# Performance work log

Hardware: AMD Instinct MI355X
Metric: run time of the kernel (lower is better)

Reference implementation:

```python
import jax, jax.numpy as jnp
import numpy as np

E = 800000
NUM_RADIAL = 6
HIDDEN = 128
OUT = 128
NUM_NODES = 50000


def setup_inputs() -> dict:
    key = jax.random.key(0)
    ks = jax.random.split(key, 12)
    x = jax.random.normal(ks[0], (E, HIDDEN), dtype=jnp.float32)
    rbf = jax.random.uniform(ks[1], (E, NUM_RADIAL), dtype=jnp.float32)
    i = jax.random.randint(ks[2], (E,), 0, NUM_NODES, dtype=jnp.int64)
    s = 1.0 / np.sqrt(HIDDEN)
    W_rbf = jax.random.normal(ks[3], (HIDDEN, NUM_RADIAL), dtype=jnp.float32) / np.sqrt(NUM_RADIAL)
    W1 = jax.random.normal(ks[4], (HIDDEN, HIDDEN), dtype=jnp.float32) * s
    b1 = jnp.zeros((HIDDEN,), dtype=jnp.float32)
    W2 = jax.random.normal(ks[5], (HIDDEN, HIDDEN), dtype=jnp.float32) * s
    b2 = jnp.zeros((HIDDEN,), dtype=jnp.float32)
    W3 = jax.random.normal(ks[6], (HIDDEN, HIDDEN), dtype=jnp.float32) * s
    b3 = jnp.zeros((HIDDEN,), dtype=jnp.float32)
    W_out = jax.random.normal(ks[7], (OUT, HIDDEN), dtype=jnp.float32) * s
    return {"x": x, "rbf": rbf, "i": i, "num_nodes": NUM_NODES,
            "W_rbf": W_rbf, "W1": W1, "b1": b1, "W2": W2, "b2": b2,
            "W3": W3, "b3": b3, "W_out": W_out}


def reference(x, rbf, i, num_nodes, W_rbf, W1, b1, W2, b2, W3, b3, W_out):
    # edge-wise: lin_rbf(rbf) * x, then scatter-add to nodes
    m = (rbf @ W_rbf.T) * x                      # [E, H]
    h = jax.ops.segment_sum(m, i, num_segments=num_nodes)  # [N, H]
    # MLP stack with swish activation
    h = jax.nn.silu(h @ W1.T + b1)
    h = jax.nn.silu(h @ W2.T + b2)
    h = jax.nn.silu(h @ W3.T + b3)
    return h @ W_out.T                           # [N, OUT]
```

## Files before the change

### kernel.cpp

```cpp
#include <hip/hip_runtime.h>

#define H 128
#define NR 6
#define MT 128
#define HS 136

typedef __attribute__((ext_vector_type(8))) short short8_t;
typedef __attribute__((ext_vector_type(4))) float f32x4;

__device__ __forceinline__ float silu_f(float v) {
    return v / (1.0f + __expf(-v));
}

__device__ __forceinline__ unsigned short bf16_rne(float f) {
    unsigned u = __float_as_uint(f);
    u += 0x7FFF + ((u >> 16) & 1);
    return (unsigned short)(u >> 16);
}
__device__ __forceinline__ float bf16_to_f(unsigned short s) {
    return __uint_as_float(((unsigned)s) << 16);
}

__global__ __launch_bounds__(256) void hist_k(const int* __restrict__ idx,
                                              int* __restrict__ counts, int E) {
    int i = blockIdx.x * 256 + threadIdx.x;
    if (i < E) atomicAdd(&counts[idx[i]], 1);
}

__global__ __launch_bounds__(1024) void scan_k(const int* __restrict__ counts,
                                               int* __restrict__ offsets, int N) {
    __shared__ int wsum[16];
    __shared__ int runv;
    const int tid = threadIdx.x, lane = tid & 63, wv = tid >> 6;
    if (tid == 0) runv = 0;
    __syncthreads();
    for (int base = 0; base < N; base += 1024) {
        const int j = base + tid;
        const int v_in = (j < N) ? counts[j] : 0;
        int v = v_in;
        #pragma unroll
        for (int d = 1; d < 64; d <<= 1) {
            int u = __shfl_up(v, d);
            if (lane >= d) v += u;
        }
        if (lane == 63) wsum[wv] = v;
        __syncthreads();
        if (tid < 16) {
            int s = wsum[tid];
            #pragma unroll
            for (int d = 1; d < 16; d <<= 1) {
                int u = __shfl_up(s, d);
                if (tid >= d) s += u;
            }
            wsum[tid] = s;
        }
        __syncthreads();
        const int wexcl = (wv == 0) ? 0 : wsum[wv - 1];
        const int r0 = runv;
        if (j < N) offsets[j] = r0 + wexcl + (v - v_in);
        const int tot = wsum[15];
        __syncthreads();
        if (tid == 0) runv = r0 + tot;
        __syncthreads();
    }
    if (tid == 0) offsets[N] = runv;
}

__global__ __launch_bounds__(256) void fill_k(const int* __restrict__ idx,
                                              const int* __restrict__ offsets,
                                              int* __restrict__ cursor,
                                              int* __restrict__ elist, int E) {
    int i = blockIdx.x * 256 + threadIdx.x;
    if (i < E) {
        int node = idx[i];
        int pos = atomicAdd(&cursor[node], 1);
        elist[offsets[node] + pos] = i;
    }
}

__global__ __launch_bounds__(256) void wsplit_k(
    const float* __restrict__ W1, const float* __restrict__ W2,
    const float* __restrict__ W3, const float* __restrict__ Wo,
    unsigned short* __restrict__ dst)
{
    const float* W = (blockIdx.y == 0) ? W1 : (blockIdx.y == 1) ? W2
                   : (blockIdx.y == 2) ? W3 : Wo;
    unsigned short* hi = dst + (size_t)blockIdx.y * 2 * H * H;
    unsigned short* lo = hi + H * H;
    const int i = (blockIdx.x * 256 + threadIdx.x) * 4;
    if (i < H * H) {
        const float4 v = *(const float4*)(W + i);
        ushort4 h4, l4;
        h4.x = bf16_rne(v.x); l4.x = bf16_rne(v.x - bf16_to_f(h4.x));
        h4.y = bf16_rne(v.y); l4.y = bf16_rne(v.y - bf16_to_f(h4.y));
        h4.z = bf16_rne(v.z); l4.z = bf16_rne(v.z - bf16_to_f(h4.z));
        h4.w = bf16_rne(v.w); l4.w = bf16_rne(v.w - bf16_to_f(h4.w));
        *(ushort4*)&hi[i] = h4;
        *(ushort4*)&lo[i] = l4;
    }
}


__device__ __forceinline__ void stage_w_pre(const unsigned short* __restrict__ g,
        unsigned short* w_hi, unsigned short* w_lo, int t)
{
    const unsigned short* hi_g = g;
    const unsigned short* lo_g = g + H * H;
    for (int i = t * 8; i < H * H; i += 4096) {
        const int c = i >> 7, k = i & 127;
        *(short8_t*)&w_hi[c * HS + k] = *(const short8_t*)&hi_g[i];
        *(short8_t*)&w_lo[c * HS + k] = *(const short8_t*)&lo_g[i];
    }
}

__device__ __forceinline__ void compute_gemm(
    const unsigned short* h_hi, const unsigned short* h_lo,
    const unsigned short* w_hi, const unsigned short* w_lo,
    const float* bl, int wv, int lr, int quad, f32x4 (&acc)[8])
{
    short8_t a_hi[4], a_lo[4];
    const int row = wv * 16 + lr;
    #pragma unroll
    for (int kb = 0; kb < 4; ++kb) {
        const int off = row * HS + kb * 32 + quad * 8;
        a_hi[kb] = *(const short8_t*)&h_hi[off];
        a_lo[kb] = *(const short8_t*)&h_lo[off];
    }
    #pragma unroll
    for (int ct = 0; ct < 8; ct += 2) {
        const int c0 = ct * 16 + lr, c1 = (ct + 1) * 16 + lr;
        const float bb0 = bl[c0], bb1 = bl[c1];
        f32x4 A0 = {bb0, bb0, bb0, bb0}, A1 = {bb1, bb1, bb1, bb1};
        short8_t b0h[4], b0l[4], b1h[4], b1l[4];
        #pragma unroll
        for (int kb = 0; kb < 4; ++kb) {
            const int o0 = c0 * HS + kb * 32 + quad * 8;
            const int o1 = c1 * HS + kb * 32 + quad * 8;
            b0h[kb] = *(const short8_t*)&w_hi[o0];
            b0l[kb] = *(const short8_t*)&w_lo[o0];
            b1h[kb] = *(const short8_t*)&w_hi[o1];
            b1l[kb] = *(const short8_t*)&w_lo[o1];
        }
        #pragma unroll
        for (int kb = 0; kb < 4; ++kb) {
            A0 = __builtin_amdgcn_mfma_f32_16x16x32_bf16(a_hi[kb], b0h[kb], A0, 0, 0, 0);
            A1 = __builtin_amdgcn_mfma_f32_16x16x32_bf16(a_hi[kb], b1h[kb], A1, 0, 0, 0);
            A0 = __builtin_amdgcn_mfma_f32_16x16x32_bf16(a_hi[kb], b0l[kb], A0, 0, 0, 0);
            A1 = __builtin_amdgcn_mfma_f32_16x16x32_bf16(a_hi[kb], b1l[kb], A1, 0, 0, 0);
            A0 = __builtin_amdgcn_mfma_f32_16x16x32_bf16(a_lo[kb], b0h[kb], A0, 0, 0, 0);
            A1 = __builtin_amdgcn_mfma_f32_16x16x32_bf16(a_lo[kb], b1h[kb], A1, 0, 0, 0);
        }
        acc[ct] = A0;
        acc[ct + 1] = A1;
    }
}

__device__ __forceinline__ void epilogue_silu(
    unsigned short* h_hi, unsigned short* h_lo,
    f32x4 (&acc)[8], int wv, int lr, int quad)
{
    #pragma unroll
    for (int ct = 0; ct < 8; ++ct)
        #pragma unroll
        for (int r = 0; r < 4; ++r) {
            const int row = wv * 16 + quad * 4 + r;
            const int col = ct * 16 + lr;
            const float v = silu_f(acc[ct][r]);
            const unsigned short hi = bf16_rne(v);
            h_hi[row * HS + col] = hi;
            h_lo[row * HS + col] = bf16_rne(v - bf16_to_f(hi));
        }
}

__global__ __launch_bounds__(512, 2) void fused_mlp(
    const float* __restrict__ x, const float* __restrict__ rbf,
    const float* __restrict__ W_rbf,
    const int* __restrict__ offsets, const int* __restrict__ elist,
    const unsigned short* __restrict__ wsp,
    const float* __restrict__ b1, const float* __restrict__ b2,
    const float* __restrict__ b3,
    float* __restrict__ out, int N)
{
    __shared__ unsigned short h_hi[H * HS], h_lo[H * HS];
    __shared__ unsigned short w_hi[H * HS], w_lo[H * HS];
    __shared__ float bl[H];

    const int t = threadIdx.x;
    const int lane = t & 63;
    const int wv = t >> 6;
    const int lr = lane & 15;
    const int quad = lane >> 4;
    const int sub = lane >> 5;
    const int l32 = lane & 31;
    const int row0 = blockIdx.x * MT;

    const float4* wp = (const float4*)(W_rbf + l32 * 24);
    const float4 w0 = wp[0], w1 = wp[1], w2 = wp[2], w3 = wp[3],
                 w4 = wp[4], w5 = wp[5];
    const float wr[4][NR] = {
        {w0.x, w0.y, w0.z, w0.w, w1.x, w1.y},
        {w1.z, w1.w, w2.x, w2.y, w2.z, w2.w},
        {w3.x, w3.y, w3.z, w3.w, w4.x, w4.y},
        {w4.z, w4.w, w5.x, w5.y, w5.z, w5.w}};

    for (int i = 0; i < 16; ++i) {
        const int node = row0 + wv * 16 + i;
        float4 ga = make_float4(0.f, 0.f, 0.f, 0.f);
        if (node < N) {
            const int beg = offsets[node], end = offsets[node + 1];
            for (int base = beg; base < end; base += 64) {
                const int cnt = min(64, end - base);
                const int e_lane = (lane < cnt) ? elist[base + lane] : 0;
                for (int p = 0; p < cnt; p += 8) {
                    int ev[4];
                    bool val[4];
                    float4 xv[4];
                    float2 rv[4][3];
                    #pragma unroll
                    for (int q = 0; q < 4; ++q) {
                        const int slot = p + 2 * q + sub;
                        val[q] = slot < cnt;
                        ev[q] = __shfl(e_lane, val[q] ? slot : cnt - 1);
                    }
                    #pragma unroll
                    for (int q = 0; q < 4; ++q) {
                        const size_t e = (size_t)ev[q];
                        xv[q] = *(const float4*)(x + e * H + l32 * 4);
                        const float2* rp = (const float2*)(rbf + e * NR);
                        rv[q][0] = rp[0]; rv[q][1] = rp[1]; rv[q][2] = rp[2];
                    }
                    #pragma unroll
                    for (int q = 0; q < 4; ++q) {
                        if (!val[q]) continue;
                        const float rr[NR] = {rv[q][0].x, rv[q][0].y, rv[q][1].x,
                                              rv[q][1].y, rv[q][2].x, rv[q][2].y};
                        float s0 = 0.f, s1 = 0.f, s2 = 0.f, s3 = 0.f;
                        #pragma unroll
                        for (int j = 0; j < NR; ++j) {
                            s0 += rr[j] * wr[0][j];
                            s1 += rr[j] * wr[1][j];
                            s2 += rr[j] * wr[2][j];
                            s3 += rr[j] * wr[3][j];
                        }
                        ga.x += s0 * xv[q].x;
                        ga.y += s1 * xv[q].y;
                        ga.z += s2 * xv[q].z;
                        ga.w += s3 * xv[q].w;
                    }
                }
            }
            ga.x += __shfl_xor(ga.x, 32);
            ga.y += __shfl_xor(ga.y, 32);
            ga.z += __shfl_xor(ga.z, 32);
            ga.w += __shfl_xor(ga.w, 32);
        }
        if (sub == 0) {
            ushort4 h4, l4;
            h4.x = bf16_rne(ga.x); l4.x = bf16_rne(ga.x - bf16_to_f(h4.x));
            h4.y = bf16_rne(ga.y); l4.y = bf16_rne(ga.y - bf16_to_f(h4.y));
            h4.z = bf16_rne(ga.z); l4.z = bf16_rne(ga.z - bf16_to_f(h4.z));
            h4.w = bf16_rne(ga.w); l4.w = bf16_rne(ga.w - bf16_to_f(h4.w));
            const int off = (wv * 16 + i) * HS + l32 * 4;
            *(ushort4*)&h_hi[off] = h4;
            *(ushort4*)&h_lo[off] = l4;
        }
    }

    stage_w_pre(wsp, w_hi, w_lo, t);
    if (t < H) bl[t] = b1[t];
    __syncthreads();

    f32x4 acc[8];

    compute_gemm(h_hi, h_lo, w_hi, w_lo, bl, wv, lr, quad, acc);
    __syncthreads();
    epilogue_silu(h_hi, h_lo, acc, wv, lr, quad);
    stage_w_pre(wsp + 32768, w_hi, w_lo, t);
    if (t < H) bl[t] = b2[t];
    __syncthreads();

    compute_gemm(h_hi, h_lo, w_hi, w_lo, bl, wv, lr, quad, acc);
    __syncthreads();
    epilogue_silu(h_hi, h_lo, acc, wv, lr, quad);
    stage_w_pre(wsp + 65536, w_hi, w_lo, t);
    if (t < H) bl[t] = b3[t];
    __syncthreads();

    compute_gemm(h_hi, h_lo, w_hi, w_lo, bl, wv, lr, quad, acc);
    __syncthreads();
    epilogue_silu(h_hi, h_lo, acc, wv, lr, quad);
    stage_w_pre(wsp + 98304, w_hi, w_lo, t);
    if (t < H) bl[t] = 0.f;
    __syncthreads();

    compute_gemm(h_hi, h_lo, w_hi, w_lo, bl, wv, lr, quad, acc);

    #pragma unroll
    for (int ct = 0; ct < 8; ++ct)
        #pragma unroll
        for (int r = 0; r < 4; ++r) {
            const int row = row0 + wv * 16 + quad * 4 + r;
            if (row < N) out[(size_t)row * H + ct * 16 + lr] = acc[ct][r];
        }
}

static inline size_t align256(size_t v) { return (v + 255) & ~(size_t)255; }

extern "C" void kernel_launch(void* const* d_in, const int* in_sizes, int n_in,
                              void* d_out, int out_size, void* d_ws, size_t ws_size,
                              hipStream_t stream) {
    const float* x     = (const float*)d_in[0];
    const float* rbf   = (const float*)d_in[1];
    const int*   idx   = (const int*)d_in[2];
    const float* W_rbf = (const float*)d_in[4];
    const float* W1    = (const float*)d_in[5];
    const float* b1    = (const float*)d_in[6];
    const float* W2    = (const float*)d_in[7];
    const float* b2    = (const float*)d_in[8];
    const float* W3    = (const float*)d_in[9];
    const float* b3    = (const float*)d_in[10];
    const float* Wo    = (const float*)d_in[11];
    float* out = (float*)d_out;

    const int E = in_sizes[0] / H;
    const int N = out_size / H;

    char* ws = (char*)d_ws;
    size_t off = 0;
    unsigned short* wsp = (unsigned short*)(ws + off);
    off = align256(off + (size_t)4 * 2 * H * H * sizeof(unsigned short));
    int* counts  = (int*)(ws + off);   off = align256(off + (size_t)N * 4);
    int* cursor  = (int*)(ws + off);   off = align256(off + (size_t)N * 4);
    int* offsets = (int*)(ws + off);   off = align256(off + (size_t)(N + 1) * 4);
    int* elist   = (int*)(ws + off);   off = align256(off + (size_t)E * 4);

    hipMemsetAsync(counts, 0, (char*)offsets - (char*)counts, stream);

    wsplit_k<<<dim3(16, 4), 256, 0, stream>>>(W1, W2, W3, Wo, wsp);
    hist_k<<<(E + 255) / 256, 256, 0, stream>>>(idx, counts, E);
    scan_k<<<1, 1024, 0, stream>>>(counts, offsets, N);
    fill_k<<<(E + 255) / 256, 256, 0, stream>>>(idx, offsets, cursor, elist, E);
    fused_mlp<<<(N + MT - 1) / MT, 512, 0, stream>>>(
        x, rbf, W_rbf, offsets, elist, wsp, b1, b2, b3, out, N);
}
```

Before: 774.4 us.

## Balance edge gather across half-waves with LDS atomics and vectorize CSR build kernels

```diff
diff --git a/kernel.cpp b/kernel.cpp
--- a/kernel.cpp
+++ b/kernel.cpp
@@ -23,8 +23,16 @@
 
 __global__ __launch_bounds__(256) void hist_k(const int* __restrict__ idx,
                                               int* __restrict__ counts, int E) {
-    int i = blockIdx.x * 256 + threadIdx.x;
-    if (i < E) atomicAdd(&counts[idx[i]], 1);
+    const int i0 = (blockIdx.x * 256 + threadIdx.x) * 4;
+    if (i0 + 3 < E) {
+        const int4 v = *(const int4*)(idx + i0);
+        atomicAdd(&counts[v.x], 1);
+        atomicAdd(&counts[v.y], 1);
+        atomicAdd(&counts[v.z], 1);
+        atomicAdd(&counts[v.w], 1);
+    } else {
+        for (int i = i0; i < E; ++i) atomicAdd(&counts[idx[i]], 1);
+    }
 }
 
 __global__ __launch_bounds__(1024) void scan_k(const int* __restrict__ counts,
@@ -34,16 +42,23 @@
     const int tid = threadIdx.x, lane = tid & 63, wv = tid >> 6;
     if (tid == 0) runv = 0;
     __syncthreads();
-    for (int base = 0; base < N; base += 1024) {
-        const int j = base + tid;
-        const int v_in = (j < N) ? counts[j] : 0;
-        int v = v_in;
+    for (int base = 0; base < N; base += 4096) {
+        const int j0 = base + tid * 4;
+        int4 v = make_int4(0, 0, 0, 0);
+        if (j0 + 3 < N) v = *(const int4*)(counts + j0);
+        else {
+            if (j0     < N) v.x = counts[j0];
+            if (j0 + 1 < N) v.y = counts[j0 + 1];
+            if (j0 + 2 < N) v.z = counts[j0 + 2];
+        }
+        const int e1 = v.x, e2 = e1 + v.y, e3 = e2 + v.z, tot = e3 + v.w;
+        int vincl = tot;
         #pragma unroll
         for (int d = 1; d < 64; d <<= 1) {
-            int u = __shfl_up(v, d);
-            if (lane >= d) v += u;
-        }
-        if (lane == 63) wsum[wv] = v;
+            int u = __shfl_up(vincl, d);
+            if (lane >= d) vincl += u;
+        }
+        if (lane == 63) wsum[wv] = vincl;
         __syncthreads();
         if (tid < 16) {
             int s = wsum[tid];
@@ -57,10 +72,17 @@
         __syncthreads();
         const int wexcl = (wv == 0) ? 0 : wsum[wv - 1];
         const int r0 = runv;
-        if (j < N) offsets[j] = r0 + wexcl + (v - v_in);
-        const int tot = wsum[15];
+        const int be = r0 + wexcl + (vincl - tot);
+        if (j0 + 3 < N) {
+            *(int4*)(offsets + j0) = make_int4(be, be + e1, be + e2, be + e3);
+        } else {
+            if (j0     < N) offsets[j0]     = be;
+            if (j0 + 1 < N) offsets[j0 + 1] = be + e1;
+            if (j0 + 2 < N) offsets[j0 + 2] = be + e2;
+        }
+        const int tottile = wsum[15];
         __syncthreads();
-        if (tid == 0) runv = r0 + tot;
+        if (tid == 0) runv = r0 + tottile;
         __syncthreads();
     }
     if (tid == 0) offsets[N] = runv;
@@ -70,11 +92,21 @@
                                               const int* __restrict__ offsets,
                                               int* __restrict__ cursor,
                                               int* __restrict__ elist, int E) {
-    int i = blockIdx.x * 256 + threadIdx.x;
-    if (i < E) {
-        int node = idx[i];
-        int pos = atomicAdd(&cursor[node], 1);
-        elist[offsets[node] + pos] = i;
+    const int i0 = (blockIdx.x * 256 + threadIdx.x) * 4;
+    if (i0 + 3 < E) {
+        const int4 v = *(const int4*)(idx + i0);
+        const int nd[4] = {v.x, v.y, v.z, v.w};
+        #pragma unroll
+        for (int q = 0; q < 4; ++q) {
+            const int pos = atomicAdd(&cursor[nd[q]], 1);
+            elist[offsets[nd[q]] + pos] = i0 + q;
+        }
+    } else {
+        for (int i = i0; i < E; ++i) {
+            const int node = idx[i];
+            const int pos = atomicAdd(&cursor[node], 1);
+            elist[offsets[node] + pos] = i;
+        }
     }
 }
 
@@ -181,9 +213,14 @@
     const float* __restrict__ b3,
     float* __restrict__ out, int N)
 {
-    __shared__ unsigned short h_hi[H * HS], h_lo[H * HS];
-    __shared__ unsigned short w_hi[H * HS], w_lo[H * HS];
+    __shared__ __align__(16) unsigned short smem[4 * H * HS];
+    unsigned short* h_hi = smem;
+    unsigned short* h_lo = smem + H * HS;
+    unsigned short* w_hi = smem + 2 * H * HS;
+    unsigned short* w_lo = smem + 3 * H * HS;
+    float* hacc = (float*)(smem + 2 * H * HS);
     __shared__ float bl[H];
+    __shared__ int off_s[MT + 1];
 
     const int t = threadIdx.x;
     const int lane = t & 63;
@@ -192,6 +229,7 @@
     const int quad = lane >> 4;
     const int sub = lane >> 5;
     const int l32 = lane & 31;
+    const int hw = t >> 5;
     const int row0 = blockIdx.x * MT;
 
     const float4* wp = (const float4*)(W_rbf + l32 * 24);
@@ -203,68 +241,126 @@
         {w3.x, w3.y, w3.z, w3.w, w4.x, w4.y},
         {w4.z, w4.w, w5.x, w5.y, w5.z, w5.w}};
 
-    for (int i = 0; i < 16; ++i) {
-        const int node = row0 + wv * 16 + i;
-        float4 ga = make_float4(0.f, 0.f, 0.f, 0.f);
-        if (node < N) {
-            const int beg = offsets[node], end = offsets[node + 1];
-            for (int base = beg; base < end; base += 64) {
-                const int cnt = min(64, end - base);
-                const int e_lane = (lane < cnt) ? elist[base + lane] : 0;
-                for (int p = 0; p < cnt; p += 8) {
-                    int ev[4];
-                    bool val[4];
-                    float4 xv[4];
-                    float2 rv[4][3];
-                    #pragma unroll
-                    for (int q = 0; q < 4; ++q) {
-                        const int slot = p + 2 * q + sub;
-                        val[q] = slot < cnt;
-                        ev[q] = __shfl(e_lane, val[q] ? slot : cnt - 1);
-                    }
-                    #pragma unroll
-                    for (int q = 0; q < 4; ++q) {
-                        const size_t e = (size_t)ev[q];
-                        xv[q] = *(const float4*)(x + e * H + l32 * 4);
-                        const float2* rp = (const float2*)(rbf + e * NR);
-                        rv[q][0] = rp[0]; rv[q][1] = rp[1]; rv[q][2] = rp[2];
-                    }
-                    #pragma unroll
-                    for (int q = 0; q < 4; ++q) {
-                        if (!val[q]) continue;
-                        const float rr[NR] = {rv[q][0].x, rv[q][0].y, rv[q][1].x,
-                                              rv[q][1].y, rv[q][2].x, rv[q][2].y};
-                        float s0 = 0.f, s1 = 0.f, s2 = 0.f, s3 = 0.f;
+    for (int i = t * 4; i < H * H; i += 2048)
+        *(float4*)&hacc[i] = make_float4(0.f, 0.f, 0.f, 0.f);
+    for (int k = t; k <= MT; k += 512)
+        off_s[k] = offsets[min(row0 + k, N)];
+    __syncthreads();
+
+    const int ebeg = off_s[0], eend = off_s[MT];
+    const int C = (eend - ebeg + 15) >> 4;
+    const int s0 = ebeg + hw * C;
+    const int e_lim = min(s0 + C, eend);
+
+    if (s0 < e_lim) {
+        int lo = 0, hi = MT;
+        while (hi - lo > 1) {
+            const int mid = (lo + hi) >> 1;
+            if (off_s[mid] <= s0) lo = mid; else hi = mid;
+        }
+        int nl = lo;
+        int nxt = off_s[nl + 1];
+        float4 acc = make_float4(0.f, 0.f, 0.f, 0.f);
+        bool dirty = false;
+
+        int eid;
+        float2 ra, rb, rc;
+        {
+            const int p = s0 + l32;
+            const int e = (p < e_lim) ? elist[p] : 0;
+            eid = e;
+            const float2* rp = (const float2*)(rbf + (size_t)e * NR);
+            ra = rp[0]; rb = rp[1]; rc = rp[2];
+        }
+
+        for (int b = s0; b < e_lim; b += 32) {
+            const int m = min(32, e_lim - b);
+            int eidN = 0;
+            float2 raN = make_float2(0.f, 0.f), rbN = raN, rcN = raN;
+            {
+                const int p = b + 32 + l32;
+                if (b + 32 < e_lim) {
+                    const int e = (p < e_lim) ? elist[p] : 0;
+                    eidN = e;
+                    const float2* rp = (const float2*)(rbf + (size_t)e * NR);
+                    raN = rp[0]; rbN = rp[1]; rcN = rp[2];
+                }
+            }
+            for (int k0 = 0; k0 < m; k0 += 4) {
+                int ee[4];
+                float rr[4][NR];
+                bool va[4];
+                #pragma unroll
+                for (int q = 0; q < 4; ++q) {
+                    const int kq = k0 + q;
+                    va[q] = kq < m;
+                    const int srcl = sub * 32 + (va[q] ? kq : 0);
+                    ee[q] = __shfl(eid, srcl);
+                    rr[q][0] = __shfl(ra.x, srcl); rr[q][1] = __shfl(ra.y, srcl);
+                    rr[q][2] = __shfl(rb.x, srcl); rr[q][3] = __shfl(rb.y, srcl);
+                    rr[q][4] = __shfl(rc.x, srcl); rr[q][5] = __shfl(rc.y, srcl);
+                }
+                float4 xv[4];
+                #pragma unroll
+                for (int q = 0; q < 4; ++q)
+                    xv[q] = *(const float4*)(x + (size_t)ee[q] * H + l32 * 4);
+                #pragma unroll
+                for (int q = 0; q < 4; ++q) {
+                    if (va[q]) {
+                        const int pos = b + k0 + q;
+                        while (pos >= nxt) {
+                            if (dirty) {
+                                float* hp = &hacc[nl * H + l32 * 4];
+                                atomicAdd(hp + 0, acc.x);
+                                atomicAdd(hp + 1, acc.y);
+                                atomicAdd(hp + 2, acc.z);
+                                atomicAdd(hp + 3, acc.w);
+                                acc = make_float4(0.f, 0.f, 0.f, 0.f);
+                                dirty = false;
+                            }
+                            ++nl;
+                            nxt = off_s[nl + 1];
+                        }
+                        float sA = 0.f, sB = 0.f, sC = 0.f, sD = 0.f;
                         #pragma unroll
                         for (int j = 0; j < NR; ++j) {
-                            s0 += rr[j] * wr[0][j];
-                            s1 += rr[j] * wr[1][j];
-                            s2 += rr[j] * wr[2][j];
-                            s3 += rr[j] * wr[3][j];
+                            sA += rr[q][j] * wr[0][j];
+                            sB += rr[q][j] * wr[1][j];
+                            sC += rr[q][j] * wr[2][j];
+                            sD += rr[q][j] * wr[3][j];
                         }
-                        ga.x += s0 * xv[q].x;
-                        ga.y += s1 * xv[q].y;
-                        ga.z += s2 * xv[q].z;
-                        ga.w += s3 * xv[q].w;
+                        acc.x += sA * xv[q].x;
+                        acc.y += sB * xv[q].y;
+                        acc.z += sC * xv[q].z;
+                        acc.w += sD * xv[q].w;
+                        dirty = true;
                     }
                 }
             }
-            ga.x += __shfl_xor(ga.x, 32);
-            ga.y += __shfl_xor(ga.y, 32);
-            ga.z += __shfl_xor(ga.z, 32);
-            ga.w += __shfl_xor(ga.w, 32);
-        }
-        if (sub == 0) {
-            ushort4 h4, l4;
-            h4.x = bf16_rne(ga.x); l4.x = bf16_rne(ga.x - bf16_to_f(h4.x));
-            h4.y = bf16_rne(ga.y); l4.y = bf16_rne(ga.y - bf16_to_f(h4.y));
-            h4.z = bf16_rne(ga.z); l4.z = bf16_rne(ga.z - bf16_to_f(h4.z));
-            h4.w = bf16_rne(ga.w); l4.w = bf16_rne(ga.w - bf16_to_f(h4.w));
-            const int off = (wv * 16 + i) * HS + l32 * 4;
-            *(ushort4*)&h_hi[off] = h4;
-            *(ushort4*)&h_lo[off] = l4;
-        }
-    }
+            eid = eidN; ra = raN; rb = rbN; rc = rcN;
+        }
+        if (dirty) {
+            float* hp = &hacc[nl * H + l32 * 4];
+            atomicAdd(hp + 0, acc.x);
+            atomicAdd(hp + 1, acc.y);
+            atomicAdd(hp + 2, acc.z);
+            atomicAdd(hp + 3, acc.w);
+        }
+    }
+    __syncthreads();
+
+    for (int i = t * 4; i < H * H; i += 2048) {
+        const float4 v = *(const float4*)&hacc[i];
+        const int r = i >> 7, k = i & 127;
+        ushort4 h4, l4;
+        h4.x = bf16_rne(v.x); l4.x = bf16_rne(v.x - bf16_to_f(h4.x));
+        h4.y = bf16_rne(v.y); l4.y = bf16_rne(v.y - bf16_to_f(h4.y));
+        h4.z = bf16_rne(v.z); l4.z = bf16_rne(v.z - bf16_to_f(h4.z));
+        h4.w = bf16_rne(v.w); l4.w = bf16_rne(v.w - bf16_to_f(h4.w));
+        *(ushort4*)&h_hi[r * HS + k] = h4;
+        *(ushort4*)&h_lo[r * HS + k] = l4;
+    }
+    __syncthreads();
 
     stage_w_pre(wsp, w_hi, w_lo, t);
     if (t < H) bl[t] = b1[t];
@@ -337,9 +433,9 @@
     hipMemsetAsync(counts, 0, (char*)offsets - (char*)counts, stream);
 
     wsplit_k<<<dim3(16, 4), 256, 0, stream>>>(W1, W2, W3, Wo, wsp);
-    hist_k<<<(E + 255) / 256, 256, 0, stream>>>(idx, counts, E);
+    hist_k<<<(E / 4 + 255) / 256, 256, 0, stream>>>(idx, counts, E);
     scan_k<<<1, 1024, 0, stream>>>(counts, offsets, N);
-    fill_k<<<(E + 255) / 256, 256, 0, stream>>>(idx, offsets, cursor, elist, E);
+    fill_k<<<(E / 4 + 255) / 256, 256, 0, stream>>>(idx, offsets, cursor, elist, E);
     fused_mlp<<<(N + MT - 1) / MT, 512, 0, stream>>>(
         x, rbf, W_rbf, offsets, elist, wsp, b1, b2, b3, out, N);
 }
```

Result: faster. 751.3 us (-3.0%).
